# Kernel tuning notes

Hardware: AMD Instinct MI355X
Metric: run time of the kernel (lower is better)

The kernel has to match this reference:

```python
import jax, jax.numpy as jnp
import numpy as np

# feature-map geometry: input 1024x1024, resnet50 stride 32
H_FM, W_FM = 32, 32
N_ANC = 9
SCALES = (2.0, 4.0, 6.0)
RATIOS = (0.5, 1.0, 1.5)
H_SCALE, W_SCALE = 32.0, 32.0  # input_size // backbone_hw
C_IN, HID = 2048, 512
BATCH = 8


def _anchor_grid():
    """Anchor boxes [H_FM, W_FM, 9, 4] in xyxy feature-map coords, clipped."""
    xs = jnp.arange(W_FM, dtype=jnp.float32) + 0.5
    ys = jnp.arange(H_FM, dtype=jnp.float32) + 0.5
    cx, cy = jnp.meshgrid(xs, ys)  # [H, W]
    ws, hs = [], []
    for s in SCALES:
        for r in RATIOS:
            ws.append(s * r)
            hs.append(s)
    ws = jnp.asarray(ws, jnp.float32)  # [9]
    hs = jnp.asarray(hs, jnp.float32)
    cx = cx[..., None]
    cy = cy[..., None]
    x1 = jnp.clip(cx - ws / 2, 0.0, float(W_FM))
    y1 = jnp.clip(cy - hs / 2, 0.0, float(H_FM))
    x2 = jnp.clip(cx + ws / 2, 0.0, float(W_FM))
    y2 = jnp.clip(cy + hs / 2, 0.0, float(H_FM))
    return jnp.stack([x1, y1, x2, y2], axis=-1)  # [H, W, 9, 4]


def _conv2d(x, w, b, pad):
    y = jax.lax.conv_general_dilated(
        x, w, window_strides=(1, 1), padding=[(pad, pad), (pad, pad)],
        dimension_numbers=('NCHW', 'OIHW', 'NCHW'))
    return y + b[None, :, None, None]


def setup_inputs() -> dict:
    key = jax.random.key(0)
    ks = jax.random.split(key, 4)

    def init(k, shape, fan_in):
        return jax.random.normal(k, shape, jnp.float32) * (1.0 / np.sqrt(fan_in))

    return {
        'feature_maps': jax.random.normal(ks[0], (BATCH, C_IN, H_FM, W_FM), jnp.float32),
        'hidden_w': init(ks[1], (HID, C_IN, 3, 3), C_IN * 9),
        'hidden_b': jnp.zeros((HID,), jnp.float32),
        'conf_w': init(ks[2], (N_ANC, HID, 1, 1), HID),
        'conf_b': jnp.zeros((N_ANC,), jnp.float32),
        'reg_w': init(ks[3], (N_ANC * 4, HID, 1, 1), HID),
        'reg_b': jnp.zeros((N_ANC * 4,), jnp.float32),
    }


def reference(feature_maps, hidden_w, hidden_b, conf_w, conf_b, reg_w, reg_b):
    # ProposalModule (eval mode: dropout is identity)
    x = jax.nn.relu(_conv2d(feature_maps, hidden_w, hidden_b, 1))    # [B,512,H,W]
    conf = _conv2d(x, conf_w, conf_b, 0).transpose(0, 2, 3, 1)       # [B,H,W,9]
    offs = _conv2d(x, reg_w, reg_b, 0).transpose(0, 2, 3, 1)         # [B,H,W,36]

    b = feature_maps.shape[0]
    scores = jax.nn.sigmoid(conf).reshape(b, -1)                     # [B, A]
    offs = offs.reshape(b, -1, 4)                                    # [B, A, 4]

    # apply (dxc, dyc, dw, dh) offsets to the anchor grid
    anc = _anchor_grid().reshape(-1, 4)                              # [A, 4]
    aw = anc[:, 2] - anc[:, 0]
    ah = anc[:, 3] - anc[:, 1]
    acx = anc[:, 0] + aw / 2
    acy = anc[:, 1] + ah / 2
    pcx = acx + offs[..., 0] * aw
    pcy = acy + offs[..., 1] * ah
    pw = aw * jnp.exp(offs[..., 2])
    ph = ah * jnp.exp(offs[..., 3])
    # proposals in image coordinates (xyxy)
    props = jnp.stack([
        (pcx - pw / 2) * W_SCALE,
        (pcy - ph / 2) * H_SCALE,
        (pcx + pw / 2) * W_SCALE,
        (pcy + ph / 2) * H_SCALE,
    ], axis=-1)                                                      # [B, A, 4]
    return jnp.concatenate([scores[..., None], props], axis=-1)      # [B, A, 5]
```

## Files before the change

### kernel.cpp

```cpp
#include <hip/hip_runtime.h>
#include <hip/hip_bf16.h>

typedef __attribute__((ext_vector_type(8))) short bf16x8;
typedef __attribute__((ext_vector_type(4))) float f32x4;

#define NPIX 8192
#define HIDC 512
#define CIN  2048

__device__ __forceinline__ ushort f2b(float f) {
    union { float f; unsigned u; } v; v.f = f;
    unsigned r = v.u + 0x7fffu + ((v.u >> 16) & 1u);
    return (ushort)(r >> 16);
}
__device__ __forceinline__ float b2f(ushort u) {
    union { unsigned u; float f; } v; v.u = ((unsigned)u) << 16; return v.f;
}

__device__ __forceinline__ void gload16(const void* g, void* l) {
    __builtin_amdgcn_global_load_lds(
        (const __attribute__((address_space(1))) void*)g,
        (__attribute__((address_space(3))) void*)l, 16, 0, 0);
}

#define WAITV0() asm volatile("s_waitcnt vmcnt(0)" ::: "memory")
#define BAR() do { asm volatile("s_barrier" ::: "memory"); \
                   __builtin_amdgcn_sched_barrier(0); } while (0)

__global__ void zero_border(ushort* __restrict__ xp) {
    int c = blockIdx.x;
    int b = blockIdx.y;
    int y, x;
    if (c < 34)      { y = 0;  x = c; }
    else if (c < 68) { y = 33; x = c - 34; }
    else if (c < 100){ y = c - 68 + 1; x = 0; }
    else             { y = c - 100 + 1; x = 33; }
    uint4* dst = (uint4*)(xp + (((size_t)b * 34 + y) * 34 + x) * CIN);
    uint4 z = {0u, 0u, 0u, 0u};
    dst[threadIdx.x] = z;
}

__global__ void pack_x(const float* __restrict__ x, ushort* __restrict__ xp) {
    __shared__ float tile[64][65];
    int b  = blockIdx.z;
    int c0 = blockIdx.y * 64;
    int p0 = blockIdx.x * 64;
    int t = threadIdx.x;
    int tx = t & 63, ty = t >> 6;
    const float* src = x + ((size_t)b * CIN + c0) * 1024 + p0;
    for (int i = ty; i < 64; i += 4)
        tile[i][tx] = src[(size_t)i * 1024 + tx];
    __syncthreads();
    int ci = t & 63, pj = t >> 6;
    for (int j = pj; j < 64; j += 4) {
        int p = p0 + j;
        int y = p >> 5, xx = p & 31;
        ushort* dst = xp + (((size_t)b * 34 + y + 1) * 34 + (xx + 1)) * CIN + c0;
        dst[ci] = f2b(tile[ci][j]);
    }
}

__global__ void pack_w(const float* __restrict__ hw, ushort* __restrict__ wpk) {
    __shared__ float ld[512 * 9];
    int n = blockIdx.x;
    int t = threadIdx.x;
    const float* src = hw + (size_t)n * (CIN * 9);
    for (int cc0 = 0; cc0 < CIN; cc0 += 512) {
        for (int i = t; i < 4608; i += 256) ld[i] = src[(size_t)cc0 * 9 + i];
        __syncthreads();
        for (int t9 = 0; t9 < 9; ++t9)
            for (int idx = t; idx < 512; idx += 256)
                wpk[((size_t)(t9 * 512 + n)) * CIN + cc0 + idx] = f2b(ld[idx * 9 + t9]);
        __syncthreads();
    }
}

__global__ void pack_w2(const float* __restrict__ cw, const float* __restrict__ rw,
                        ushort* __restrict__ w2b) {
    int i = blockIdx.x * 256 + threadIdx.x;
    if (i >= 48 * 512) return;
    int m = i >> 9, c = i & 511;
    float v = 0.f;
    if (m < 9) v = cw[m * 512 + c];
    else if (m < 45) v = rw[(m - 9) * 512 + c];
    w2b[i] = f2b(v);
}

#define NT_TILES 72
#define KSPLIT   4608

__launch_bounds__(512, 2)
__global__ void conv_gemm_splitk(const ushort* __restrict__ xp, const ushort* __restrict__ wpk,
                                 ushort* __restrict__ pp) {
    __shared__ __align__(16) ushort A0[256 * 64];
    __shared__ __align__(16) ushort B0[256 * 64];
    __shared__ __align__(16) ushort A1[256 * 64];
    __shared__ __align__(16) ushort B1[256 * 64];

    int t = threadIdx.x;

    int bid = blockIdx.x;
    int xcd = bid & 7;
    int nt = xcd & 1, ks = xcd >> 1;
    int mt = bid >> 3;
    int pix0 = mt * 256, n0 = nt * 256;

    int w = t >> 6, l = t & 63;
    int wr = w >> 2;
    int wc = w & 3;

    int r0 = t >> 3;
    int dOff = ((t & 7) ^ (r0 & 7)) * 8;

    int aRowBase[4];
#pragma unroll
    for (int j = 0; j < 4; ++j) {
        int p = pix0 + r0 + 64 * j;
        int b = p >> 10, py = (p >> 5) & 31, px = p & 31;
        aRowBase[j] = ((b * 34 + py) * 34 + px) * CIN;
    }
    int bRowBase[4];
#pragma unroll
    for (int j = 0; j < 4; ++j)
        bRowBase[j] = (n0 + r0 + 64 * j) * CIN;

    int ksBase = ks * KSPLIT;

    f32x4 zero = {0.f, 0.f, 0.f, 0.f};
    f32x4 acc[8][4];
#pragma unroll
    for (int i = 0; i < 8; ++i)
#pragma unroll
        for (int j = 0; j < 4; ++j) acc[i][j] = zero;

    int lr = l & 15;
    int swz0 = ((l >> 4) ^ (lr & 7)) * 16;
    int swz1 = ((4 + (l >> 4)) ^ (lr & 7)) * 16;
    int abase = (wr * 128 + lr) * 128;
    int bbase = (wc * 64 + lr) * 128;

    auto stageA = [&](int kt, ushort* As) {
        int fk = ksBase + kt * 64;
        int tap = fk >> 11, chc = fk & 2047;
        int dy = tap / 3, dx = tap - dy * 3;
        int aoff = (dy * 34 + dx) * CIN + chc + dOff;
#pragma unroll
        for (int j = 0; j < 4; ++j)
            gload16(xp + aRowBase[j] + aoff, (char*)As + (t + 512 * j) * 16);
    };
    auto stageB = [&](int kt, ushort* Bs) {
        int fk = ksBase + kt * 64;
        int tap = fk >> 11, chc = fk & 2047;
        int boff = tap * (512 * CIN) + chc + dOff;
#pragma unroll
        for (int j = 0; j < 4; ++j)
            gload16(wpk + bRowBase[j] + boff, (char*)Bs + (t + 512 * j) * 16);
    };

    bf16x8 af[4], bf0[4], bf1[4];

    auto ldA = [&](const ushort* As, int mh, int sz) {
#pragma unroll
        for (int m = 0; m < 4; ++m)
            af[m] = *(const bf16x8*)((const char*)As + abase + (mh * 4 + m) * 2048 + sz);
    };
    auto ldB = [&](const ushort* Bs, int sz, bf16x8* bf) {
#pragma unroll
        for (int ni = 0; ni < 4; ++ni)
            bf[ni] = *(const bf16x8*)((const char*)Bs + bbase + ni * 2048 + sz);
    };
    auto mm = [&](int mh, const bf16x8* bf) {
        __builtin_amdgcn_s_setprio(1);
#pragma unroll
        for (int m = 0; m < 4; ++m)
#pragma unroll
            for (int ni = 0; ni < 4; ++ni)
                acc[mh * 4 + m][ni] = __builtin_amdgcn_mfma_f32_16x16x32_bf16(
                    af[m], bf[ni], acc[mh * 4 + m][ni], 0, 0, 0);
        __builtin_amdgcn_s_setprio(0);
    };

    auto tile = [&](int i, ushort* Ac, ushort* Bc, ushort* An, ushort* Bn) {
        bool st = (i + 1 < NT_TILES);
        WAITV0(); BAR();
        ldB(Bc, swz0, bf0); ldA(Ac, 0, swz0);
        if (st) stageA(i + 1, An);
        BAR();
        mm(0, bf0);
        BAR();
        ldA(Ac, 1, swz0);
        if (st) stageB(i + 1, Bn);
        BAR();
        mm(1, bf0);
        BAR();
        ldB(Bc, swz1, bf1); ldA(Ac, 0, swz1);
        BAR();
        mm(0, bf1);
        BAR();
        ldA(Ac, 1, swz1);
        BAR();
        mm(1, bf1);
    };

    stageA(0, A0); stageB(0, B0);
    for (int i = 0; i < NT_TILES; i += 2) {
        tile(i,     A0, B0, A1, B1);
        tile(i + 1, A1, B1, A0, B0);
    }

    ushort* dst = pp + (size_t)ks * (NPIX * HIDC);
    int hi = l >> 4;
#pragma unroll
    for (int mi = 0; mi < 8; ++mi) {
#pragma unroll
        for (int ni = 0; ni < 4; ++ni) {
            int col = n0 + wc * 64 + ni * 16 + lr;
#pragma unroll
            for (int r = 0; r < 4; ++r) {
                int row = pix0 + wr * 128 + mi * 16 + hi * 4 + r;
                dst[(size_t)row * HIDC + col] = f2b(acc[mi][ni][r]);
            }
        }
    }
}

__global__ void reduce_bias_relu(const ushort* __restrict__ pp, const float* __restrict__ hb,
                                 ushort* __restrict__ hidden) {
    int i = blockIdx.x * 256 + threadIdx.x;
    const size_t S = (size_t)NPIX * HIDC;
    bf16x8 p0 = *(const bf16x8*)(pp + (size_t)i * 8);
    bf16x8 p1 = *(const bf16x8*)(pp + S + (size_t)i * 8);
    bf16x8 p2 = *(const bf16x8*)(pp + 2 * S + (size_t)i * 8);
    bf16x8 p3 = *(const bf16x8*)(pp + 3 * S + (size_t)i * 8);
    int col0 = (i & 63) * 8;
    bf16x8 r;
#pragma unroll
    for (int j = 0; j < 8; ++j) {
        float v = b2f((ushort)p0[j]) + b2f((ushort)p1[j]) +
                  b2f((ushort)p2[j]) + b2f((ushort)p3[j]) + hb[col0 + j];
        r[j] = (short)f2b(v > 0.f ? v : 0.f);
    }
    *(bf16x8*)(hidden + (size_t)i * 8) = r;
}

#define NKSTEP 576

__launch_bounds__(256, 1)
__global__ void conv_gemm(const ushort* __restrict__ xp, const ushort* __restrict__ wpk,
                          const float* __restrict__ hb, ushort* __restrict__ hidden) {
    __shared__ __align__(16) ushort A0[128 * 32];
    __shared__ __align__(16) ushort B0[128 * 32];
    __shared__ __align__(16) ushort A1[128 * 32];
    __shared__ __align__(16) ushort B1[128 * 32];

    int t = threadIdx.x;
    int orig = blockIdx.x;
    int xcd = orig & 7;
    int ix  = orig >> 3;
    int nb  = ix & 3;
    int pb  = (xcd << 3) + (ix >> 2);
    int n0   = nb * 128;
    int pix0 = pb * 128;

    int w = t >> 6, l = t & 63;
    int wr = w >> 1, wc = w & 1;

    int u  = t ^ ((t >> 3) & 7);
    int rA = u >> 2;
    int kA = (u & 3) * 8;

    int p1 = pix0 + rA, p2 = p1 + 64;
    int b   = p1 >> 10;
    int py1 = (p1 >> 5) & 31, px1 = p1 & 31;
    int py2 = (p2 >> 5) & 31, px2 = p2 & 31;

    size_t aBase1 = ((size_t)b * 34 + py1) * 34 + px1;
    size_t aBase2 = ((size_t)b * 34 + py2) * 34 + px2;

    f32x4 zero = {0.f, 0.f, 0.f, 0.f};
    f32x4 acc[4][4];
#pragma unroll
    for (int i = 0; i < 4; ++i)
#pragma unroll
        for (int j = 0; j < 4; ++j) acc[i][j] = zero;

    int lr = l & 15;
    int kc = l >> 4;
    int sw = ((lr * 4 + kc) ^ ((lr >> 1) & 7)) * 16;

    auto stage = [&](int kk, ushort* As, ushort* Bs) {
        int tap = kk >> 6;
        int c0 = (kk & 63) << 5;
        int dy = tap / 3, dx = tap - dy * 3;
        size_t aoff = (size_t)(dy * 34 + dx) * CIN + kA + c0;
        gload16(xp + aBase1 * CIN + aoff, (char*)As + t * 16);
        gload16(xp + aBase2 * CIN + aoff, (char*)As + 4096 + t * 16);
        const ushort* bp = wpk + ((size_t)(tap * 512) + n0 + rA) * CIN + kA + c0;
        gload16(bp, (char*)Bs + t * 16);
        gload16(bp + (size_t)64 * CIN, (char*)Bs + 4096 + t * 16);
    };

    auto compute = [&](const ushort* As, const ushort* Bs) {
        const char* ab = (const char*)As + wr * 4096 + sw;
        const char* bb = (const char*)Bs + wc * 4096 + sw;
        bf16x8 af[4], bfr[4];
#pragma unroll
        for (int mi = 0; mi < 4; ++mi)
            af[mi] = *(const bf16x8*)(ab + mi * 1024);
#pragma unroll
        for (int ni = 0; ni < 4; ++ni)
            bfr[ni] = *(const bf16x8*)(bb + ni * 1024);
#pragma unroll
        for (int mi = 0; mi < 4; ++mi)
#pragma unroll
            for (int ni = 0; ni < 4; ++ni)
                acc[mi][ni] = __builtin_amdgcn_mfma_f32_16x16x32_bf16(
                    af[mi], bfr[ni], acc[mi][ni], 0, 0, 0);
    };

    stage(0, A0, B0);
    __syncthreads();
    for (int kk = 0; kk < NKSTEP; kk += 2) {
        if (kk + 1 < NKSTEP) stage(kk + 1, A1, B1);
        compute(A0, B0);
        __syncthreads();
        if (kk + 2 < NKSTEP) stage(kk + 2, A0, B0);
        compute(A1, B1);
        __syncthreads();
    }

    int lr4 = (l >> 4) * 4;
#pragma unroll
    for (int mi = 0; mi < 4; ++mi) {
#pragma unroll
        for (int ni = 0; ni < 4; ++ni) {
            int col = n0 + wc * 64 + ni * 16 + lr;
            float bias = hb[col];
#pragma unroll
            for (int r = 0; r < 4; ++r) {
                int row = pix0 + wr * 64 + mi * 16 + lr4 + r;
                float v = acc[mi][ni][r] + bias;
                v = v > 0.f ? v : 0.f;
                hidden[(size_t)row * HIDC + col] = f2b(v);
            }
        }
    }
}

__launch_bounds__(256)
__global__ void gemm2(const ushort* __restrict__ hidden, const ushort* __restrict__ w2b,
                      const float* __restrict__ cb, const float* __restrict__ rb,
                      float* __restrict__ g) {
    __shared__ __align__(16) ushort W2[48 * 520];
    int t = threadIdx.x;
    const unsigned* src = (const unsigned*)w2b;
    unsigned* dstW = (unsigned*)&W2[0];
    for (int i = t; i < 12288; i += 256) {
        int m = i >> 8, c2 = i & 255;
        dstW[m * 260 + c2] = src[i];
    }
    __syncthreads();
    int w = t >> 6, l = t & 63;
    int p0 = blockIdx.x * 64 + w * 16;
    int lr = l & 15, lk = (l >> 4) * 8;
    f32x4 zero = {0.f, 0.f, 0.f, 0.f};
    f32x4 acc[3] = {zero, zero, zero};
    const ushort* hrow = hidden + (size_t)(p0 + lr) * HIDC + lk;
#pragma unroll 4
    for (int k0 = 0; k0 < 16; ++k0) {
        bf16x8 a = *(const bf16x8*)(hrow + k0 * 32);
#pragma unroll
        for (int ni = 0; ni < 3; ++ni) {
            bf16x8 bb = *(const bf16x8*)&W2[(ni * 16 + lr) * 520 + k0 * 32 + lk];
            acc[ni] = __builtin_amdgcn_mfma_f32_16x16x32_bf16(a, bb, acc[ni], 0, 0, 0);
        }
    }
    int lr4 = (l >> 4) * 4;
#pragma unroll
    for (int ni = 0; ni < 3; ++ni) {
        int m = ni * 16 + lr;
        float bias = (m < 9) ? cb[m] : ((m < 45) ? rb[m - 9] : 0.f);
#pragma unroll
        for (int r = 0; r < 4; ++r) {
            int p = p0 + lr4 + r;
            g[(size_t)p * 48 + m] = acc[ni][r] + bias;
        }
    }
}

__global__ void proposals(const float* __restrict__ g, float* __restrict__ out) {
    int i = blockIdx.x * 256 + threadIdx.x;
    if (i >= NPIX * 9) return;
    int p = i / 9, a = i - p * 9;
    int y = (p >> 5) & 31, x = p & 31;
    int si = a / 3, ri = a - si * 3;
    float hA = 2.f * (float)(si + 1);
    float wA = (float)((si + 1) * (ri + 1));

    const float* gp = g + (size_t)p * 48;
    float conf = gp[a];
    float o0 = gp[9 + a * 4 + 0];
    float o1 = gp[9 + a * 4 + 1];
    float o2 = gp[9 + a * 4 + 2];
    float o3 = gp[9 + a * 4 + 3];

    float cx = x + 0.5f, cy = y + 0.5f;
    float x1 = fminf(fmaxf(cx - wA * 0.5f, 0.f), 32.f);
    float y1 = fminf(fmaxf(cy - hA * 0.5f, 0.f), 32.f);
    float x2 = fminf(fmaxf(cx + wA * 0.5f, 0.f), 32.f);
    float y2 = fminf(fmaxf(cy + hA * 0.5f, 0.f), 32.f);
    float aw = x2 - x1, ah = y2 - y1;
    float acx = x1 + aw * 0.5f, acy = y1 + ah * 0.5f;
    float pcx = acx + o0 * aw, pcy = acy + o1 * ah;
    float pw = aw * expf(o2), ph = ah * expf(o3);
    float s = 1.f / (1.f + expf(-conf));

    float* o = out + (size_t)i * 5;
    o[0] = s;
    o[1] = (pcx - pw * 0.5f) * 32.f;
    o[2] = (pcy - ph * 0.5f) * 32.f;
    o[3] = (pcx + pw * 0.5f) * 32.f;
    o[4] = (pcy + ph * 0.5f) * 32.f;
}

extern "C" void kernel_launch(void* const* d_in, const int* in_sizes, int n_in,
                              void* d_out, int out_size, void* d_ws, size_t ws_size,
                              hipStream_t stream) {
    const float* x  = (const float*)d_in[0];
    const float* hw = (const float*)d_in[1];
    const float* hb = (const float*)d_in[2];
    const float* cw = (const float*)d_in[3];
    const float* cb = (const float*)d_in[4];
    const float* rw = (const float*)d_in[5];
    const float* rb = (const float*)d_in[6];
    float* out = (float*)d_out;

    char* ws = (char*)d_ws;
    ushort* xp     = (ushort*)(ws);
    ushort* wpk    = (ushort*)(ws + 37879808);
    ushort* hidden = (ushort*)(ws + 56754176);
    ushort* w2b    = (ushort*)(ws + 65142784);
    float*  g      = (float*)(ws + 65191936);
    ushort* pp     = (ushort*)(ws + 66764800);
    const size_t WS_NEED_SPLITK = 66764800 + 33554432;

    hipLaunchKernelGGL(zero_border, dim3(132, 8), dim3(256), 0, stream, xp);
    hipLaunchKernelGGL(pack_x, dim3(16, 32, 8), dim3(256), 0, stream, x, xp);
    hipLaunchKernelGGL(pack_w, dim3(512), dim3(256), 0, stream, hw, wpk);
    hipLaunchKernelGGL(pack_w2, dim3(96), dim3(256), 0, stream, cw, rw, w2b);
    if (ws_size >= WS_NEED_SPLITK) {
        hipLaunchKernelGGL(conv_gemm_splitk, dim3(256), dim3(512), 0, stream, xp, wpk, pp);
        hipLaunchKernelGGL(reduce_bias_relu, dim3(2048), dim3(256), 0, stream, pp, hb, hidden);
    } else {
        hipLaunchKernelGGL(conv_gemm, dim3(256), dim3(256), 0, stream, xp, wpk, hb, hidden);
    }
    hipLaunchKernelGGL(gemm2, dim3(128), dim3(256), 0, stream, hidden, w2b, cb, rb, g);
    hipLaunchKernelGGL(proposals, dim3(288), dim3(256), 0, stream, g, out);
}
```

Before: 211.1 us.

## Fuse split-K reduce+bias+ReLU into head GEMM and drop intra-tile barriers

The split-K partial sums are now reduced, biased and ReLU'd inside the 1x1 head GEMM's A-operand load, removing the separate reduce kernel and the round-trip of the hidden activation through memory. The conv GEMM main loop replaces most s_barrier calls with compiler scheduling barriers only, letting waves progress independently within a tile. The trade-offs are a head GEMM now reading four partial buffers with a small grid, and weaker synchronisation between waves sharing LDS.

```diff
diff --git a/kernel.cpp b/kernel.cpp
--- a/kernel.cpp
+++ b/kernel.cpp
@@ -26,6 +26,7 @@
 #define WAITV0() asm volatile("s_waitcnt vmcnt(0)" ::: "memory")
 #define BAR() do { asm volatile("s_barrier" ::: "memory"); \
                    __builtin_amdgcn_sched_barrier(0); } while (0)
+#define SCHED() __builtin_amdgcn_sched_barrier(0)
 
 __global__ void zero_border(ushort* __restrict__ xp) {
     int c = blockIdx.x;
@@ -185,21 +186,22 @@
         WAITV0(); BAR();
         ldB(Bc, swz0, bf0); ldA(Ac, 0, swz0);
         if (st) stageA(i + 1, An);
-        BAR();
+        SCHED();
         mm(0, bf0);
-        BAR();
+        SCHED();
         ldA(Ac, 1, swz0);
         if (st) stageB(i + 1, Bn);
-        BAR();
+        SCHED();
         mm(1, bf0);
-        BAR();
+        SCHED();
         ldB(Bc, swz1, bf1); ldA(Ac, 0, swz1);
-        BAR();
+        SCHED();
         mm(0, bf1);
-        BAR();
+        SCHED();
         ldA(Ac, 1, swz1);
-        BAR();
+        SCHED();
         mm(1, bf1);
+        SCHED();
     };
 
     stageA(0, A0); stageB(0, B0);
@@ -222,25 +224,6 @@
             }
         }
     }
-}
-
-__global__ void reduce_bias_relu(const ushort* __restrict__ pp, const float* __restrict__ hb,
-                                 ushort* __restrict__ hidden) {
-    int i = blockIdx.x * 256 + threadIdx.x;
-    const size_t S = (size_t)NPIX * HIDC;
-    bf16x8 p0 = *(const bf16x8*)(pp + (size_t)i * 8);
-    bf16x8 p1 = *(const bf16x8*)(pp + S + (size_t)i * 8);
-    bf16x8 p2 = *(const bf16x8*)(pp + 2 * S + (size_t)i * 8);
-    bf16x8 p3 = *(const bf16x8*)(pp + 3 * S + (size_t)i * 8);
-    int col0 = (i & 63) * 8;
-    bf16x8 r;
-#pragma unroll
-    for (int j = 0; j < 8; ++j) {
-        float v = b2f((ushort)p0[j]) + b2f((ushort)p1[j]) +
-                  b2f((ushort)p2[j]) + b2f((ushort)p3[j]) + hb[col0 + j];
-        r[j] = (short)f2b(v > 0.f ? v : 0.f);
-    }
-    *(bf16x8*)(hidden + (size_t)i * 8) = r;
 }
 
 #define NKSTEP 576
@@ -343,6 +326,59 @@
                 v = v > 0.f ? v : 0.f;
                 hidden[(size_t)row * HIDC + col] = f2b(v);
             }
+        }
+    }
+}
+
+__launch_bounds__(256)
+__global__ void gemm2f(const ushort* __restrict__ pp, const float* __restrict__ hb,
+                       const ushort* __restrict__ w2b,
+                       const float* __restrict__ cb, const float* __restrict__ rb,
+                       float* __restrict__ g) {
+    __shared__ __align__(16) ushort W2[48 * 520];
+    int t = threadIdx.x;
+    const unsigned* src = (const unsigned*)w2b;
+    unsigned* dstW = (unsigned*)&W2[0];
+    for (int i = t; i < 12288; i += 256) {
+        int m = i >> 8, c2 = i & 255;
+        dstW[m * 260 + c2] = src[i];
+    }
+    __syncthreads();
+    int w = t >> 6, l = t & 63;
+    int p0 = blockIdx.x * 64 + w * 16;
+    int lr = l & 15, lk = (l >> 4) * 8;
+    const size_t S = (size_t)NPIX * HIDC;
+    f32x4 zero = {0.f, 0.f, 0.f, 0.f};
+    f32x4 acc[3] = {zero, zero, zero};
+    const ushort* hrow = pp + (size_t)(p0 + lr) * HIDC + lk;
+#pragma unroll 4
+    for (int k0 = 0; k0 < 16; ++k0) {
+        bf16x8 a0 = *(const bf16x8*)(hrow + k0 * 32);
+        bf16x8 a1 = *(const bf16x8*)(hrow + S + k0 * 32);
+        bf16x8 a2 = *(const bf16x8*)(hrow + 2 * S + k0 * 32);
+        bf16x8 a3 = *(const bf16x8*)(hrow + 3 * S + k0 * 32);
+        bf16x8 a;
+#pragma unroll
+        for (int j = 0; j < 8; ++j) {
+            float v = b2f((ushort)a0[j]) + b2f((ushort)a1[j]) +
+                      b2f((ushort)a2[j]) + b2f((ushort)a3[j]) + hb[k0 * 32 + lk + j];
+            a[j] = (short)f2b(v > 0.f ? v : 0.f);
+        }
+#pragma unroll
+        for (int ni = 0; ni < 3; ++ni) {
+            bf16x8 bb = *(const bf16x8*)&W2[(ni * 16 + lr) * 520 + k0 * 32 + lk];
+            acc[ni] = __builtin_amdgcn_mfma_f32_16x16x32_bf16(a, bb, acc[ni], 0, 0, 0);
+        }
+    }
+    int lr4 = (l >> 4) * 4;
+#pragma unroll
+    for (int ni = 0; ni < 3; ++ni) {
+        int m = ni * 16 + lr;
+        float bias = (m < 9) ? cb[m] : ((m < 45) ? rb[m - 9] : 0.f);
+#pragma unroll
+        for (int r = 0; r < 4; ++r) {
+            int p = p0 + lr4 + r;
+            g[(size_t)p * 48 + m] = acc[ni][r] + bias;
         }
     }
 }
@@ -450,10 +486,10 @@
     hipLaunchKernelGGL(pack_w2, dim3(96), dim3(256), 0, stream, cw, rw, w2b);
     if (ws_size >= WS_NEED_SPLITK) {
         hipLaunchKernelGGL(conv_gemm_splitk, dim3(256), dim3(512), 0, stream, xp, wpk, pp);
-        hipLaunchKernelGGL(reduce_bias_relu, dim3(2048), dim3(256), 0, stream, pp, hb, hidden);
+        hipLaunchKernelGGL(gemm2f, dim3(128), dim3(256), 0, stream, pp, hb, w2b, cb, rb, g);
     } else {
         hipLaunchKernelGGL(conv_gemm, dim3(256), dim3(256), 0, stream, xp, wpk, hb, hidden);
-    }
-    hipLaunchKernelGGL(gemm2, dim3(128), dim3(256), 0, stream, hidden, w2b, cb, rb, g);
+        hipLaunchKernelGGL(gemm2, dim3(128), dim3(256), 0, stream, hidden, w2b, cb, rb, g);
+    }
     hipLaunchKernelGGL(proposals, dim3(288), dim3(256), 0, stream, g, out);
 }
```

After: 191.3 us. 9.4% less time.
